# Kernel optimization log

Hardware: AMD Instinct MI355X
Metric: run time of the kernel (lower is better)

## Reference

```python
import jax, jax.numpy as jnp
import numpy as np

B, N, D = 8, 2048, 256
BIG = 1e9  # max_int_value used to mask the diagonal
LN_EPS = 1e-5  # F.layer_norm default eps


def setup_inputs() -> dict:
    key = jax.random.key(0)
    kq, kk = jax.random.split(key)
    q = jax.random.normal(kq, (B, N, D), dtype=jnp.float32)
    k = jax.random.normal(kk, (B, N, D), dtype=jnp.float32)
    return {"q": q, "k": k, "top_k_instances": 100, "top_k_relationships": 5}


def _forward(q, k, K, R):
    b, n, d = q.shape
    # dense QK^T + softmax over keys -> (b, n, n)
    scores1 = jax.nn.softmax(jnp.einsum('bid,bjd->bij', q, k), axis=-1)
    # instance selection: top-K of the softmaxed diagonal, sorted ascending
    diag = jnp.diagonal(scores1, axis1=-2, axis2=-1)           # (b, n)
    top_idx = jnp.sort(jax.lax.top_k(diag, K)[1], axis=-1)      # (b, K)
    # gather selected rows then selected columns -> (b, K, K)
    sel = jnp.take_along_axis(scores1, top_idx[:, :, None], axis=1)   # (b, K, n)
    rel = jnp.take_along_axis(sel, jnp.broadcast_to(top_idx[:, None, :], (b, K, K)), axis=2)
    # mask diagonal with BIG (masked_fill_ with eye)
    rel = jnp.where(jnp.eye(K, dtype=bool)[None], BIG, rel)
    # top-R relationships per selected instance; torch recovers them via
    # scatter(-1)+where, which yields row-major order with ascending column
    # indices inside each row -> equivalent to sorting top-k indices per row.
    rel_idx = jnp.sort(jax.lax.top_k(rel, R)[1], axis=-1)       # (b, K, R)
    rows = jnp.broadcast_to(jnp.arange(K)[:, None], (K, R)).reshape(-1)  # (K*R,)
    subj = top_idx[:, rows]                                     # (b, K*R) original subject ids
    obj = jnp.take_along_axis(top_idx, rel_idx.reshape(b, K * R), axis=-1)  # (b, K*R)
    batch_ids = jnp.broadcast_to(jnp.arange(b)[:, None], (b, K * R))
    soi = jnp.stack([batch_ids, subj, obj], axis=-1)            # (b, K*R, 3)
    # gather embeddings from q and layer-norm (no affine)
    se = jnp.take_along_axis(q, subj[:, :, None], axis=1)       # (b, K*R, d)
    oe = jnp.take_along_axis(q, obj[:, :, None], axis=1)
    re = se + oe
    mu = jnp.mean(re, axis=-1, keepdims=True)
    var = jnp.var(re, axis=-1, keepdims=True)
    re = (re - mu) * jax.lax.rsqrt(var + LN_EPS)
    return scores1, soi, re


def reference(q, k, top_k_instances, top_k_relationships):
    return _forward(q, k, top_k_instances, top_k_relationships)
```

## Files before the change

### kernel.cpp

```cpp
#include <hip/hip_runtime.h>
#include <math.h>

#define BB 8
#define NN 2048
#define DD 256
#define KK 100
#define RR 5
#define BIGV 1000000000.0f
#define LN_EPS 1e-5f

typedef __attribute__((ext_vector_type(8))) short short8;
typedef __attribute__((ext_vector_type(4))) float floatx4;

__device__ static inline unsigned short f2bf_rne(float x) {
  unsigned int u = __float_as_uint(x);
  unsigned int r = (u + 0x7FFFu + ((u >> 16) & 1u)) >> 16;
  return (unsigned short)r;
}
__device__ static inline float bf2f(unsigned short h) {
  return __uint_as_float(((unsigned int)h) << 16);
}

__device__ static inline void gl_lds16(const unsigned short* g, unsigned short* l) {
  __builtin_amdgcn_global_load_lds(
      (const __attribute__((address_space(1))) unsigned int*)(g),
      (__attribute__((address_space(3))) unsigned int*)(l), 16, 0, 0);
}

__global__ __launch_bounds__(256) void split_bf16(const float* __restrict__ q,
                                                  const float* __restrict__ k,
                                                  ushort4* __restrict__ qhi,
                                                  ushort4* __restrict__ qlo,
                                                  ushort4* __restrict__ khi,
                                                  ushort4* __restrict__ klo) {
  const int n4 = BB * NN * DD / 4;
  const float4* src = (blockIdx.y == 0) ? (const float4*)q : (const float4*)k;
  ushort4* hi = blockIdx.y ? khi : qhi;
  ushort4* lo = blockIdx.y ? klo : qlo;
  for (int i = blockIdx.x * 256 + threadIdx.x; i < n4; i += gridDim.x * 256) {
    float4 v = src[i];
    ushort4 h, l;
    h.x = f2bf_rne(v.x); l.x = f2bf_rne(v.x - bf2f(h.x));
    h.y = f2bf_rne(v.y); l.y = f2bf_rne(v.y - bf2f(h.y));
    h.z = f2bf_rne(v.z); l.z = f2bf_rne(v.z - bf2f(h.z));
    h.w = f2bf_rne(v.w); l.w = f2bf_rne(v.w - bf2f(h.w));
    hi[i] = h; lo[i] = l;
  }
}

__global__ __launch_bounds__(256, 3) void gemm_mfma_split(
    const unsigned short* __restrict__ qhi, const unsigned short* __restrict__ qlo,
    const unsigned short* __restrict__ khi, const unsigned short* __restrict__ klo,
    float* __restrict__ s) {
  __shared__ unsigned short lds[2][2][8][512];

  const int lid = blockIdx.x + ((blockIdx.y + (blockIdx.z << 4)) << 4);
  const int swz = ((lid & 7) << 8) + (lid >> 3);
  const int bx = swz & 15;
  const int by = (swz >> 4) & 15;
  const int b = swz >> 8;
  const int i0 = by * 128, j0 = bx * 128;

  const int t = threadIdx.x;
  const int w = t >> 6, L = t & 63;
  const int wx = w & 1, wy = w >> 1;
  const int q_ = L >> 4, m_ = L & 15;

  const size_t bofs = (size_t)b * NN * DD;

  const unsigned short* gah = qhi + bofs + (size_t)(i0 + wy * 64 + m_) * DD + q_ * 8;
  const unsigned short* gal = qlo + bofs + (size_t)(i0 + wy * 64 + m_) * DD + q_ * 8;

  const unsigned short* gb0;
  const unsigned short* gb1;
  const unsigned short* gb2;
  const unsigned short* gb3;
#define MKB(u, dst)                                                          \
  {                                                                          \
    int f = w * 4 + (u);                                                     \
    const unsigned short* pl = (f < 8) ? khi : klo;                          \
    int ft = f & 7;                                                          \
    dst = pl + bofs + (size_t)(j0 + ft * 16 + m_) * DD + q_ * 8;             \
  }
  MKB(0, gb0) MKB(1, gb1) MKB(2, gb2) MKB(3, gb3)
#undef MKB

#define STAGE(buf, kb0)                                                      \
  do {                                                                       \
    gl_lds16(gb0 + (kb0), &lds[buf][(w * 4 + 0) >> 3][(w * 4 + 0) & 7][0]);  \
    gl_lds16(gb1 + (kb0), &lds[buf][(w * 4 + 1) >> 3][(w * 4 + 1) & 7][0]);  \
    gl_lds16(gb2 + (kb0), &lds[buf][(w * 4 + 2) >> 3][(w * 4 + 2) & 7][0]);  \
    gl_lds16(gb3 + (kb0), &lds[buf][(w * 4 + 3) >> 3][(w * 4 + 3) & 7][0]);  \
  } while (0)

  floatx4 acc[4][4];
#pragma unroll
  for (int i = 0; i < 4; ++i)
#pragma unroll
    for (int j = 0; j < 4; ++j) acc[i][j] = (floatx4){0.f, 0.f, 0.f, 0.f};

  STAGE(0, 0);
  int cur = 0;
#pragma unroll
  for (int it = 0; it < 8; ++it) {
    const int kb0 = it * 32;
    short8 ah[4], al[4];
#pragma unroll
    for (int i = 0; i < 4; ++i) {
      ah[i] = *(const short8*)(gah + (size_t)i * 16 * DD + kb0);
      al[i] = *(const short8*)(gal + (size_t)i * 16 * DD + kb0);
    }
    asm volatile("" ::: "memory");
    if (it < 7) {
      STAGE(cur ^ 1, kb0 + 32);
      asm volatile("s_waitcnt vmcnt(4)" ::: "memory");
    } else {
      asm volatile("s_waitcnt vmcnt(0)" ::: "memory");
    }
    __builtin_amdgcn_s_barrier();

    short8 bh[4], bl[4];
#pragma unroll
    for (int j = 0; j < 4; ++j) {
      bh[j] = *(const short8*)&lds[cur][0][wx * 4 + j][L * 8];
      bl[j] = *(const short8*)&lds[cur][1][wx * 4 + j][L * 8];
    }
    __builtin_amdgcn_s_setprio(1);
#pragma unroll
    for (int i = 0; i < 4; ++i)
#pragma unroll
      for (int j = 0; j < 4; ++j) {
        acc[i][j] = __builtin_amdgcn_mfma_f32_16x16x32_bf16(ah[i], bh[j], acc[i][j], 0, 0, 0);
        acc[i][j] = __builtin_amdgcn_mfma_f32_16x16x32_bf16(ah[i], bl[j], acc[i][j], 0, 0, 0);
        acc[i][j] = __builtin_amdgcn_mfma_f32_16x16x32_bf16(al[i], bh[j], acc[i][j], 0, 0, 0);
      }
    __builtin_amdgcn_s_setprio(0);
    __builtin_amdgcn_s_barrier();
    cur ^= 1;
  }
#undef STAGE

#pragma unroll
  for (int i = 0; i < 4; ++i)
#pragma unroll
    for (int j = 0; j < 4; ++j)
#pragma unroll
      for (int r = 0; r < 4; ++r) {
        int row = i0 + wy * 64 + i * 16 + q_ * 4 + r;
        int col = j0 + wx * 64 + j * 16 + m_;
        s[((size_t)b * NN + row) * NN + col] = acc[i][j][r];
      }
}

__global__ __launch_bounds__(256) void gemm_logits(const float* __restrict__ q,
                                                   const float* __restrict__ k,
                                                   float* __restrict__ s) {
  __shared__ float As[32][132];
  __shared__ float Bs[32][132];
  const int b = blockIdx.z;
  const int i0 = blockIdx.y * 128;
  const int j0 = blockIdx.x * 128;
  const int t = threadIdx.x;
  const int tx = t & 15;
  const int ty = t >> 4;
  const float* qb = q + (size_t)b * NN * DD;
  const float* kb = k + (size_t)b * NN * DD;

  float acc[8][8];
#pragma unroll
  for (int i = 0; i < 8; ++i)
#pragma unroll
    for (int j = 0; j < 8; ++j) acc[i][j] = 0.f;

  for (int kb0 = 0; kb0 < DD; kb0 += 32) {
#pragma unroll
    for (int l = 0; l < 4; ++l) {
      int f = l * 256 + t;
      int row = f >> 3;
      int c4 = (f & 7) * 4;
      float4 va = *(const float4*)(qb + (size_t)(i0 + row) * DD + kb0 + c4);
      float4 vb = *(const float4*)(kb + (size_t)(j0 + row) * DD + kb0 + c4);
      As[c4 + 0][row] = va.x; As[c4 + 1][row] = va.y;
      As[c4 + 2][row] = va.z; As[c4 + 3][row] = va.w;
      Bs[c4 + 0][row] = vb.x; Bs[c4 + 1][row] = vb.y;
      Bs[c4 + 2][row] = vb.z; Bs[c4 + 3][row] = vb.w;
    }
    __syncthreads();
#pragma unroll
    for (int kk = 0; kk < 32; ++kk) {
      float a[8], bv[8];
      *(float4*)&a[0] = *(const float4*)&As[kk][ty * 8];
      *(float4*)&a[4] = *(const float4*)&As[kk][ty * 8 + 4];
      *(float4*)&bv[0] = *(const float4*)&Bs[kk][tx * 8];
      *(float4*)&bv[4] = *(const float4*)&Bs[kk][tx * 8 + 4];
#pragma unroll
      for (int i = 0; i < 8; ++i)
#pragma unroll
        for (int j = 0; j < 8; ++j) acc[i][j] += a[i] * bv[j];
    }
    __syncthreads();
  }

#pragma unroll
  for (int i = 0; i < 8; ++i) {
    size_t row = (size_t)(i0 + ty * 8 + i);
    float* po = s + ((size_t)b * NN + row) * NN + j0 + tx * 8;
    *(float4*)po = make_float4(acc[i][0], acc[i][1], acc[i][2], acc[i][3]);
    *(float4*)(po + 4) = make_float4(acc[i][4], acc[i][5], acc[i][6], acc[i][7]);
  }
}

__device__ inline float pick4(float4 v, int j) {
  return j == 0 ? v.x : (j == 1 ? v.y : (j == 2 ? v.z : v.w));
}

__global__ __launch_bounds__(256) void softmax_rows(float* __restrict__ s,
                                                    float* __restrict__ diag) {
  const int bi = blockIdx.x;
  const int irow = bi & (NN - 1);
  const int t = threadIdx.x;
  float4* rowp = (float4*)(s + (size_t)bi * NN);
  float4 v0 = rowp[t];
  float4 v1 = rowp[256 + t];

  __shared__ float red[4];
  float m = fmaxf(fmaxf(fmaxf(v0.x, v0.y), fmaxf(v0.z, v0.w)),
                  fmaxf(fmaxf(v1.x, v1.y), fmaxf(v1.z, v1.w)));
#pragma unroll
  for (int off = 32; off; off >>= 1) m = fmaxf(m, __shfl_xor(m, off));
  if ((t & 63) == 0) red[t >> 6] = m;
  __syncthreads();
  m = fmaxf(fmaxf(red[0], red[1]), fmaxf(red[2], red[3]));
  __syncthreads();

  float4 e0, e1;
  e0.x = expf(v0.x - m); e0.y = expf(v0.y - m);
  e0.z = expf(v0.z - m); e0.w = expf(v0.w - m);
  e1.x = expf(v1.x - m); e1.y = expf(v1.y - m);
  e1.z = expf(v1.z - m); e1.w = expf(v1.w - m);
  float sum = e0.x + e0.y + e0.z + e0.w + e1.x + e1.y + e1.z + e1.w;
#pragma unroll
  for (int off = 32; off; off >>= 1) sum += __shfl_xor(sum, off);
  if ((t & 63) == 0) red[t >> 6] = sum;
  __syncthreads();
  sum = red[0] + red[1] + red[2] + red[3];

  float inv = 1.0f / sum;
  float4 s0 = make_float4(e0.x * inv, e0.y * inv, e0.z * inv, e0.w * inv);
  float4 s1 = make_float4(e1.x * inv, e1.y * inv, e1.z * inv, e1.w * inv);
  rowp[t] = s0;
  rowp[256 + t] = s1;

  int c0 = t * 4;
  if (irow >= c0 && irow < c0 + 4) diag[bi] = pick4(s0, irow - c0);
  int c1 = 1024 + t * 4;
  if (irow >= c1 && irow < c1 + 4) diag[bi] = pick4(s1, irow - c1);
}

__global__ __launch_bounds__(256) void topk_rank(const float* __restrict__ diag,
                                                 unsigned char* __restrict__ flags) {
  const int b = blockIdx.y;
  const int c = blockIdx.x;
  const int t = threadIdx.x;
  __shared__ unsigned long long key[NN];
  __shared__ unsigned short partial[256];

#pragma unroll
  for (int sIt = 0; sIt < 8; ++sIt) {
    int i = t + sIt * 256;
    unsigned int vb = __float_as_uint(diag[b * NN + i]);
    key[i] = ((unsigned long long)vb << 32) | (unsigned int)(NN - 1 - i);
  }
  __syncthreads();

  const int e = c * 128 + (t & 127);
  const int base = (t >> 7) * 1024;
  const unsigned long long my = key[e];
  int r = 0;
#pragma unroll 8
  for (int j = 0; j < 1024; ++j) r += (key[base + j] > my) ? 1 : 0;
  partial[t] = (unsigned short)r;
  __syncthreads();

  if (t < 128) {
    int rank = (int)partial[t] + (int)partial[t + 128];
    flags[b * NN + e] = (rank < KK) ? 1 : 0;
  }
}

__global__ __launch_bounds__(1024) void topk_compact(const unsigned char* __restrict__ flags,
                                                     int* __restrict__ topidx) {
  const int b = blockIdx.x;
  const int t = threadIdx.x;
  __shared__ unsigned long long mask[32];
  const bool f0 = flags[b * NN + t] != 0;
  const bool f1 = flags[b * NN + t + 1024] != 0;
  const unsigned long long m0 = __ballot(f0);
  const unsigned long long m1 = __ballot(f1);
  const int w = t >> 6, l = t & 63;
  if (l == 0) { mask[w] = m0; mask[16 + w] = m1; }
  __syncthreads();
  if (f0) {
    int pos = __popcll(m0 & ((1ull << l) - 1ull));
    for (int j = 0; j < w; ++j) pos += __popcll(mask[j]);
    topidx[b * KK + pos] = t;
  }
  if (f1) {
    int pos = __popcll(m1 & ((1ull << l) - 1ull));
    for (int j = 0; j < 16 + w; ++j) pos += __popcll(mask[j]);
    topidx[b * KK + pos] = t + 1024;
  }
}

__global__ __launch_bounds__(64) void rel_topk(const float* __restrict__ s,
                                               const int* __restrict__ topidx,
                                               float* __restrict__ soi,
                                               int2* __restrict__ pairs) {
  const int b = blockIdx.y;
  const int i = blockIdx.x;
  const int l = threadIdx.x;
  const int* tixb = topidx + b * KK;
  const int subj = tixb[i];
  const float* srow = s + ((size_t)b * NN + subj) * NN;

  const int j0 = l, j1 = l + 64;
  int c0 = tixb[j0];
  float v0 = (j0 == i) ? BIGV : srow[c0];
  unsigned long long k0 =
      ((unsigned long long)__float_as_uint(v0) << 32) | (unsigned int)(KK - 1 - j0);
  unsigned long long k1 = 0ull;
  if (j1 < KK) {
    int c1 = tixb[j1];
    float v1 = (j1 == i) ? BIGV : srow[c1];
    k1 = ((unsigned long long)__float_as_uint(v1) << 32) | (unsigned int)(KK - 1 - j1);
  }

  int sel[RR];
#pragma unroll
  for (int r = 0; r < RR; ++r) {
    unsigned long long best = k0 > k1 ? k0 : k1;
#pragma unroll
    for (int off = 32; off; off >>= 1) {
      unsigned long long o = __shfl_xor(best, off);
      if (o > best) best = o;
    }
    int js = KK - 1 - (int)(unsigned int)(best & 0xFFFFFFFFull);
    sel[r] = js;
    if (j0 == js) k0 = 0ull;
    if (j1 == js) k1 = 0ull;
  }

  if (l == 0) {
#pragma unroll
    for (int a2 = 0; a2 < RR; ++a2)
#pragma unroll
      for (int b2 = a2 + 1; b2 < RR; ++b2)
        if (sel[b2] < sel[a2]) { int tmp = sel[a2]; sel[a2] = sel[b2]; sel[b2] = tmp; }
#pragma unroll
    for (int r = 0; r < RR; ++r) {
      int obj = tixb[sel[r]];
      size_t p = ((size_t)b * KK + i) * RR + r;
      soi[p * 3 + 0] = (float)b;
      soi[p * 3 + 1] = (float)subj;
      soi[p * 3 + 2] = (float)obj;
      pairs[p] = make_int2(subj, obj);
    }
  }
}

__global__ __launch_bounds__(64) void edge_ln(const float* __restrict__ q,
                                              const int2* __restrict__ pairs,
                                              float* __restrict__ re) {
  const int p = blockIdx.x;
  const int b = p / (KK * RR);
  const int l = threadIdx.x;
  int2 pr = pairs[p];
  const float4* qs = (const float4*)(q + ((size_t)b * NN + pr.x) * DD);
  const float4* qo = (const float4*)(q + ((size_t)b * NN + pr.y) * DD);
  float4 a = qs[l];
  float4 o = qo[l];
  a.x += o.x; a.y += o.y; a.z += o.z; a.w += o.w;
  float sum = a.x + a.y + a.z + a.w;
  float sq = a.x * a.x + a.y * a.y + a.z * a.z + a.w * a.w;
#pragma unroll
  for (int off = 32; off; off >>= 1) {
    sum += __shfl_xor(sum, off);
    sq += __shfl_xor(sq, off);
  }
  float mu = sum * (1.f / DD);
  float var = sq * (1.f / DD) - mu * mu;
  float rs = rsqrtf(var + LN_EPS);
  float4 r4 = make_float4((a.x - mu) * rs, (a.y - mu) * rs,
                          (a.z - mu) * rs, (a.w - mu) * rs);
  ((float4*)(re + (size_t)p * DD))[l] = r4;
}

extern "C" void kernel_launch(void* const* d_in, const int* in_sizes, int n_in,
                              void* d_out, int out_size, void* d_ws, size_t ws_size,
                              hipStream_t stream) {
  const float* q = (const float*)d_in[0];
  const float* k = (const float*)d_in[1];

  float* out = (float*)d_out;
  float* scores = out;
  float* soi = out + (size_t)BB * NN * NN;
  float* re = soi + (size_t)BB * KK * RR * 3;

  char* ws = (char*)d_ws;
  float* diag = (float*)ws;
  int* topidx = (int*)(ws + (size_t)BB * NN * 4);
  int2* pairs = (int2*)(ws + (size_t)BB * NN * 4 + (size_t)BB * KK * 4);
  unsigned char* flags =
      (unsigned char*)(ws + (size_t)BB * NN * 4 + (size_t)BB * KK * 4 +
                       (size_t)BB * KK * RR * 8);
  const size_t small_end = 128 * 1024;
  const size_t plane = (size_t)BB * NN * DD * 2;
  const bool use_mfma = ws_size >= small_end + 4 * plane;

  if (use_mfma) {
    unsigned short* qhi = (unsigned short*)(ws + small_end);
    unsigned short* qlo = (unsigned short*)(ws + small_end + plane);
    unsigned short* khi = (unsigned short*)(ws + small_end + 2 * plane);
    unsigned short* klo = (unsigned short*)(ws + small_end + 3 * plane);
    split_bf16<<<dim3(1024, 2), 256, 0, stream>>>(q, k, (ushort4*)qhi, (ushort4*)qlo,
                                                  (ushort4*)khi, (ushort4*)klo);
    gemm_mfma_split<<<dim3(NN / 128, NN / 128, BB), 256, 0, stream>>>(qhi, qlo, khi, klo,
                                                                      scores);
  } else {
    gemm_logits<<<dim3(NN / 128, NN / 128, BB), 256, 0, stream>>>(q, k, scores);
  }
  softmax_rows<<<dim3(BB * NN), 256, 0, stream>>>(scores, diag);
  topk_rank<<<dim3(16, BB), 256, 0, stream>>>(diag, flags);
  topk_compact<<<dim3(BB), 1024, 0, stream>>>(flags, topidx);
  rel_topk<<<dim3(KK, BB), 64, 0, stream>>>(scores, topidx, soi, pairs);
  edge_ln<<<dim3(BB * KK * RR), 64, 0, stream>>>(q, pairs, re);
}
```

Before: 311.5 us.

## Deepen GEMM prefetch to two stages and fuse relationship top-k with edge layernorm

The split-bf16 MFMA GEMM now keeps two K-slices in flight. Both the B tile in LDS and the A fragments in registers are double-buffered, and the next-next slice is issued right after each compute step. The launch-bounds occupancy hint drops from 3 to 2 to leave room for the extra registers. Separately, the relationship top-k kernel now computes the edge layer-norm for its five pairs directly, which removes the edge_ln launch and the pairs round-trip through workspace and reuses the subject row. The risks are lower occupancy and higher register pressure in the GEMM.

```diff
diff --git a/kernel.cpp b/kernel.cpp
--- a/kernel.cpp
+++ b/kernel.cpp
@@ -48,7 +48,7 @@
   }
 }
 
-__global__ __launch_bounds__(256, 3) void gemm_mfma_split(
+__global__ __launch_bounds__(256, 2) void gemm_mfma_split(
     const unsigned short* __restrict__ qhi, const unsigned short* __restrict__ qlo,
     const unsigned short* __restrict__ khi, const unsigned short* __restrict__ klo,
     float* __restrict__ s) {
@@ -93,27 +93,45 @@
     gl_lds16(gb3 + (kb0), &lds[buf][(w * 4 + 3) >> 3][(w * 4 + 3) & 7][0]);  \
   } while (0)
 
+#define ALOAD(dh, dl, kb0)                                                   \
+  do {                                                                       \
+    _Pragma("unroll") for (int i = 0; i < 4; ++i) {                          \
+      dh[i] = *(const short8*)(gah + (size_t)i * 16 * DD + (kb0));           \
+      dl[i] = *(const short8*)(gal + (size_t)i * 16 * DD + (kb0));           \
+    }                                                                        \
+  } while (0)
+
+#define COMPUTE(AH, AL)                                                      \
+  do {                                                                       \
+    _Pragma("unroll") for (int i = 0; i < 4; ++i)                            \
+        _Pragma("unroll") for (int j = 0; j < 4; ++j) {                      \
+      acc[i][j] = __builtin_amdgcn_mfma_f32_16x16x32_bf16(AH[i], bh[j],      \
+                                                          acc[i][j], 0, 0, 0);\
+      acc[i][j] = __builtin_amdgcn_mfma_f32_16x16x32_bf16(AH[i], bl[j],      \
+                                                          acc[i][j], 0, 0, 0);\
+      acc[i][j] = __builtin_amdgcn_mfma_f32_16x16x32_bf16(AL[i], bh[j],      \
+                                                          acc[i][j], 0, 0, 0);\
+    }                                                                        \
+  } while (0)
+
   floatx4 acc[4][4];
 #pragma unroll
   for (int i = 0; i < 4; ++i)
 #pragma unroll
     for (int j = 0; j < 4; ++j) acc[i][j] = (floatx4){0.f, 0.f, 0.f, 0.f};
 
+  short8 a0h[4], a0l[4], a1h[4], a1l[4];
+
   STAGE(0, 0);
-  int cur = 0;
+  ALOAD(a0h, a0l, 0);
+  STAGE(1, 32);
+  ALOAD(a1h, a1l, 32);
+
 #pragma unroll
   for (int it = 0; it < 8; ++it) {
-    const int kb0 = it * 32;
-    short8 ah[4], al[4];
-#pragma unroll
-    for (int i = 0; i < 4; ++i) {
-      ah[i] = *(const short8*)(gah + (size_t)i * 16 * DD + kb0);
-      al[i] = *(const short8*)(gal + (size_t)i * 16 * DD + kb0);
-    }
-    asm volatile("" ::: "memory");
-    if (it < 7) {
-      STAGE(cur ^ 1, kb0 + 32);
-      asm volatile("s_waitcnt vmcnt(4)" ::: "memory");
+    const int cur = it & 1;
+    if (it < 6) {
+      asm volatile("s_waitcnt vmcnt(12)" ::: "memory");
     } else {
       asm volatile("s_waitcnt vmcnt(0)" ::: "memory");
     }
@@ -125,20 +143,17 @@
       bh[j] = *(const short8*)&lds[cur][0][wx * 4 + j][L * 8];
       bl[j] = *(const short8*)&lds[cur][1][wx * 4 + j][L * 8];
     }
-    __builtin_amdgcn_s_setprio(1);
-#pragma unroll
-    for (int i = 0; i < 4; ++i)
-#pragma unroll
-      for (int j = 0; j < 4; ++j) {
-        acc[i][j] = __builtin_amdgcn_mfma_f32_16x16x32_bf16(ah[i], bh[j], acc[i][j], 0, 0, 0);
-        acc[i][j] = __builtin_amdgcn_mfma_f32_16x16x32_bf16(ah[i], bl[j], acc[i][j], 0, 0, 0);
-        acc[i][j] = __builtin_amdgcn_mfma_f32_16x16x32_bf16(al[i], bh[j], acc[i][j], 0, 0, 0);
-      }
-    __builtin_amdgcn_s_setprio(0);
+    if (cur == 0) COMPUTE(a0h, a0l); else COMPUTE(a1h, a1l);
     __builtin_amdgcn_s_barrier();
-    cur ^= 1;
+    if (it < 6) {
+      STAGE(cur, (it + 2) * 32);
+      if (cur == 0) ALOAD(a0h, a0l, (it + 2) * 32);
+      else          ALOAD(a1h, a1l, (it + 2) * 32);
+    }
   }
 #undef STAGE
+#undef ALOAD
+#undef COMPUTE
 
 #pragma unroll
   for (int i = 0; i < 4; ++i)
@@ -312,10 +327,11 @@
   }
 }
 
-__global__ __launch_bounds__(64) void rel_topk(const float* __restrict__ s,
-                                               const int* __restrict__ topidx,
-                                               float* __restrict__ soi,
-                                               int2* __restrict__ pairs) {
+__global__ __launch_bounds__(64) void rel_topk_ln(const float* __restrict__ s,
+                                                  const int* __restrict__ topidx,
+                                                  const float* __restrict__ q,
+                                                  float* __restrict__ soi,
+                                                  float* __restrict__ re) {
   const int b = blockIdx.y;
   const int i = blockIdx.x;
   const int l = threadIdx.x;
@@ -350,49 +366,44 @@
     if (j1 == js) k1 = 0ull;
   }
 
-  if (l == 0) {
-#pragma unroll
-    for (int a2 = 0; a2 < RR; ++a2)
-#pragma unroll
-      for (int b2 = a2 + 1; b2 < RR; ++b2)
-        if (sel[b2] < sel[a2]) { int tmp = sel[a2]; sel[a2] = sel[b2]; sel[b2] = tmp; }
-#pragma unroll
-    for (int r = 0; r < RR; ++r) {
-      int obj = tixb[sel[r]];
-      size_t p = ((size_t)b * KK + i) * RR + r;
-      soi[p * 3 + 0] = (float)b;
-      soi[p * 3 + 1] = (float)subj;
-      soi[p * 3 + 2] = (float)obj;
-      pairs[p] = make_int2(subj, obj);
-    }
-  }
-}
-
-__global__ __launch_bounds__(64) void edge_ln(const float* __restrict__ q,
-                                              const int2* __restrict__ pairs,
-                                              float* __restrict__ re) {
-  const int p = blockIdx.x;
-  const int b = p / (KK * RR);
-  const int l = threadIdx.x;
-  int2 pr = pairs[p];
-  const float4* qs = (const float4*)(q + ((size_t)b * NN + pr.x) * DD);
-  const float4* qo = (const float4*)(q + ((size_t)b * NN + pr.y) * DD);
-  float4 a = qs[l];
-  float4 o = qo[l];
-  a.x += o.x; a.y += o.y; a.z += o.z; a.w += o.w;
-  float sum = a.x + a.y + a.z + a.w;
-  float sq = a.x * a.x + a.y * a.y + a.z * a.z + a.w * a.w;
-#pragma unroll
-  for (int off = 32; off; off >>= 1) {
-    sum += __shfl_xor(sum, off);
-    sq += __shfl_xor(sq, off);
-  }
-  float mu = sum * (1.f / DD);
-  float var = sq * (1.f / DD) - mu * mu;
-  float rs = rsqrtf(var + LN_EPS);
-  float4 r4 = make_float4((a.x - mu) * rs, (a.y - mu) * rs,
-                          (a.z - mu) * rs, (a.w - mu) * rs);
-  ((float4*)(re + (size_t)p * DD))[l] = r4;
+#pragma unroll
+  for (int a2 = 0; a2 < RR; ++a2)
+#pragma unroll
+    for (int b2 = a2 + 1; b2 < RR; ++b2)
+      if (sel[b2] < sel[a2]) { int tmp = sel[a2]; sel[a2] = sel[b2]; sel[b2] = tmp; }
+
+  if (l < RR) {
+    int obj = tixb[sel[l]];
+    size_t p = ((size_t)b * KK + i) * RR + l;
+    soi[p * 3 + 0] = (float)b;
+    soi[p * 3 + 1] = (float)subj;
+    soi[p * 3 + 2] = (float)obj;
+  }
+
+  const float4* qs = (const float4*)(q + ((size_t)b * NN + subj) * DD);
+  const float4 a0 = qs[l];
+#pragma unroll
+  for (int r = 0; r < RR; ++r) {
+    int obj = tixb[sel[r]];
+    const float4* qo = (const float4*)(q + ((size_t)b * NN + obj) * DD);
+    float4 a = a0;
+    float4 o = qo[l];
+    a.x += o.x; a.y += o.y; a.z += o.z; a.w += o.w;
+    float sum = a.x + a.y + a.z + a.w;
+    float sq = a.x * a.x + a.y * a.y + a.z * a.z + a.w * a.w;
+#pragma unroll
+    for (int off = 32; off; off >>= 1) {
+      sum += __shfl_xor(sum, off);
+      sq += __shfl_xor(sq, off);
+    }
+    float mu = sum * (1.f / DD);
+    float var = sq * (1.f / DD) - mu * mu;
+    float rs = rsqrtf(var + LN_EPS);
+    float4 r4 = make_float4((a.x - mu) * rs, (a.y - mu) * rs,
+                            (a.z - mu) * rs, (a.w - mu) * rs);
+    size_t p = ((size_t)b * KK + i) * RR + r;
+    ((float4*)(re + p * DD))[l] = r4;
+  }
 }
 
 extern "C" void kernel_launch(void* const* d_in, const int* in_sizes, int n_in,
@@ -409,7 +420,6 @@
   char* ws = (char*)d_ws;
   float* diag = (float*)ws;
   int* topidx = (int*)(ws + (size_t)BB * NN * 4);
-  int2* pairs = (int2*)(ws + (size_t)BB * NN * 4 + (size_t)BB * KK * 4);
   unsigned char* flags =
       (unsigned char*)(ws + (size_t)BB * NN * 4 + (size_t)BB * KK * 4 +
                        (size_t)BB * KK * RR * 8);
@@ -432,6 +442,5 @@
   softmax_rows<<<dim3(BB * NN), 256, 0, stream>>>(scores, diag);
   topk_rank<<<dim3(16, BB), 256, 0, stream>>>(diag, flags);
   topk_compact<<<dim3(BB), 1024, 0, stream>>>(flags, topidx);
-  rel_topk<<<dim3(KK, BB), 64, 0, stream>>>(scores, topidx, soi, pairs);
-  edge_ln<<<dim3(BB * KK * RR), 64, 0, stream>>>(q, pairs, re);
-}
+  rel_topk_ln<<<dim3(KK, BB), 64, 0, stream>>>(scores, topidx, q, soi, re);
+}
```

Result: no change. 308.2 us (-1.0%).
